# Kernel tuning notes

Hardware: AMD Instinct MI355X
Metric: run time of the kernel (lower is better)

Reference implementation:

```python
import jax, jax.numpy as jnp
import numpy as np

# ---- configuration (matches init_kwargs) ----
IH, IW, IC, OC = 32, 32, 8, 16
KH = KW = 3
STRIDE = (1, 1)
PAD = (1, 1)
DIL = (1, 1)
P = 5                       # num_gp_pts per GP neuron
I_DIM = IC * KH * KW        # 72 = kernel_input_size
OH = (IH + 2 * PAD[0] - DIL[0] * (KH - 1) - 1) // STRIDE[0] + 1
OW = (IW + 2 * PAD[1] - DIL[1] * (KW - 1) - 1) // STRIDE[1] + 1
JITTER = 1e-4


def setup_inputs() -> dict:
    key = jax.random.key(0)
    k1, k2, k3, k4, k5 = jax.random.split(key, 5)
    N = 8
    x_mean = jax.random.normal(k1, (N, IH, IW, IC), jnp.float32)
    # variances must be positive
    x_var = 0.1 + 0.9 * jax.random.uniform(k2, (N, IH, IW, IC), jnp.float32)
    # inducing inputs: spread on [-1,1] with small perturbation (well-conditioned K)
    base = jnp.linspace(-1.0, 1.0, P, dtype=jnp.float32)
    z = base[None, None, :] + 0.05 * jax.random.normal(k3, (OC, I_DIM, P), jnp.float32)
    h = jax.random.normal(k4, (OC, I_DIM, P), jnp.float32)      # inducing outputs
    raw_l = jax.random.uniform(k5, (OC, I_DIM), jnp.float32)    # pre-softplus lengthscale
    return {"x_mean": x_mean, "x_var": x_var, "z": z, "h": h, "raw_l": raw_l}


def im2col(img):
    """[N,IH,IW,C] NHWC -> [N*L, C*KH*KW], torch.nn.Unfold ordering (channel slowest)."""
    x = jnp.transpose(img, (0, 3, 1, 2))  # NCHW, matches the torch transposes
    patches = jax.lax.conv_general_dilated_patches(
        x, (KH, KW), STRIDE, [(PAD[0], PAD[0]), (PAD[1], PAD[1])], rhs_dilation=DIL
    )  # [N, C*KH*KW, OH, OW], feature dim channel-major like torch unfold
    Nb = patches.shape[0]
    return patches.reshape(Nb, I_DIM, OH * OW).transpose(0, 2, 1).reshape(Nb * OH * OW, I_DIM)


def gp_layer(mu, s2, z, h, raw_l):
    """GP-neuron (KAN-style) moment propagation.
    mu, s2: [R, I]; z, h: [O, I, P]; raw_l: [O, I].
    Per neuron (o,i): SE kernel k(a,b)=exp(-(a-b)^2/(2 l^2)), unit signal variance.
    Under x_i ~ N(mu_i, s2_i):
      q_p   = sqrt(l^2/(l^2+s2)) * exp(-(mu-z_p)^2 / (2 (l^2+s2)))   (expected kernel)
      mean  = q . K^{-1} h
      var   = 1 - q . K^{-1} q
    Layer output (KAN sum over inputs): y_o = sum_i f_oi(x_i).
    """
    l2 = jax.nn.softplus(raw_l) ** 2                                  # [O,I]
    dz = z[:, :, :, None] - z[:, :, None, :]                          # [O,I,P,P]
    K = jnp.exp(-0.5 * dz**2 / l2[:, :, None, None]) + JITTER * jnp.eye(P, dtype=mu.dtype)
    Kinv = jnp.linalg.inv(K)                                          # [O,I,P,P] (tiny)
    alpha = jnp.einsum('oipq,oiq->oip', Kinv, h)                      # [O,I,P]

    d = l2[None, :, :, None] + s2[:, None, :, None]                   # [R,O,I,1]
    diff = mu[:, None, :, None] - z[None]                             # [R,O,I,P]
    q = jnp.sqrt(l2[None, :, :, None] / d) * jnp.exp(-0.5 * diff**2 / d)  # [R,O,I,P]

    out_mean = jnp.einsum('roip,oip->ro', q, alpha)                   # [R,O]
    qK = jnp.einsum('roip,oipq->roiq', q, Kinv)                       # [R,O,I,P]
    qKq = jnp.einsum('roiq,roiq->ro', qK, q)                          # [R,O]
    # sum_i (k(x,x) - q K^{-1} q) with k(x,x)=1 -> I - sum_i qKq_i
    out_var = jnp.maximum(jnp.asarray(mu.shape[1], mu.dtype) - qKq, 1e-6)
    return out_mean, out_var


def reference(x_mean, x_var, z, h, raw_l):
    N = x_mean.shape[0]
    mu = im2col(x_mean)                  # [N*L, I]
    s2 = im2col(x_var)                   # [N*L, I]
    m, v = gp_layer(mu, s2, z, h, raw_l)
    # col2im: [N*L, OC] -> [N, OH, OW, OC]
    return m.reshape(N, OH, OW, OC), v.reshape(N, OH, OW, OC)
```

## Files before the change

kernel.cpp:

```cpp
#include <hip/hip_runtime.h>
#include <math.h>

#define OC_N   16
#define I_DIM  72
#define PN     5
#define NEU    (OC_N * I_DIM)
#define NF     32
#define RTOT   8192
#define OUT_HALF (RTOT * OC_N)
#define LOG2E  1.4426950408889634f
#define RLOG2E 0.6931471805599453f

#if __has_builtin(__builtin_amdgcn_rcpf)
#define RCPF(x) __builtin_amdgcn_rcpf(x)
#else
#define RCPF(x) (1.0f / (x))
#endif
#if __has_builtin(__builtin_amdgcn_exp2f)
#define EXP2F(x) __builtin_amdgcn_exp2f(x)
#else
#define EXP2F(x) exp2f(x)
#endif
#if __has_builtin(__builtin_amdgcn_logf)
#define LOG2F(x) __builtin_amdgcn_logf(x)
#else
#define LOG2F(x) log2f(x)
#endif
#if __has_builtin(__builtin_amdgcn_rsqf)
#define RSQF(x) __builtin_amdgcn_rsqf(x)
#else
#define RSQF(x) rsqrtf(x)
#endif


__global__ __launch_bounds__(256) void gp_prep_kernel(
    const float* __restrict__ zin, const float* __restrict__ hin,
    const float* __restrict__ rlin, float* __restrict__ nr) {
  int idx = blockIdx.x * blockDim.x + threadIdx.x;
  if (idx >= NEU) return;
  float x  = rlin[idx];
  float t  = EXP2F(-fabsf(x) * LOG2E);
  float sp = fmaxf(x, 0.0f) + LOG2F(1.0f + t) * RLOG2E;
  float l2 = sp * sp;
  float cexp = -0.5f * LOG2E * RCPF(l2);

  float zz[PN], hh[PN];
#pragma unroll
  for (int p = 0; p < PN; ++p) {
    zz[p] = zin[idx * PN + p];
    hh[p] = hin[idx * PN + p];
  }
  float A[PN][PN], B[PN][PN];
#pragma unroll
  for (int p = 0; p < PN; ++p) {
#pragma unroll
    for (int q = 0; q < PN; ++q) {
      float dz = zz[p] - zz[q];
      A[p][q] = EXP2F(cexp * dz * dz);
      B[p][q] = (p == q) ? 1.0f : 0.0f;
    }
  }
#pragma unroll
  for (int p = 0; p < PN; ++p) A[p][p] += 1e-4f;

#pragma unroll
  for (int c = 0; c < PN; ++c) {
    float pivinv = RCPF(A[c][c]);
#pragma unroll
    for (int j = 0; j < PN; ++j) { A[c][j] *= pivinv; B[c][j] *= pivinv; }
#pragma unroll
    for (int r = 0; r < PN; ++r) {
      if (r == c) continue;
      float f = A[r][c];
#pragma unroll
      for (int j = 0; j < PN; ++j) { A[r][j] -= f * A[c][j]; B[r][j] -= f * B[c][j]; }
    }
  }
  float alpha[PN];
#pragma unroll
  for (int p = 0; p < PN; ++p) {
    float s = 0.0f;
#pragma unroll
    for (int q = 0; q < PN; ++q) s += B[p][q] * hh[q];
    alpha[p] = s;
  }
  float* o = nr + idx * NF;
  o[0] = l2;
  o[1] = 0.0f;
#pragma unroll
  for (int p = 0; p < PN; ++p) {
    o[2 + p]  = zz[p];
    o[7 + p]  = alpha[p];
    o[12 + p] = B[p][p];
  }
  int j = 17;
#pragma unroll
  for (int p = 0; p < PN; ++p)
#pragma unroll
    for (int q = p + 1; q < PN; ++q) o[j++] = 2.0f * B[p][q];
  o[27] = o[28] = o[29] = o[30] = o[31] = 0.0f;
}

__global__ __launch_bounds__(256, 2) void gp_main_kernel(
    const float* __restrict__ xm, const float* __restrict__ xv,
    const float* __restrict__ nr, float2* __restrict__ pmq) {
  const int tx   = threadIdx.x;
  const int lane = tx & 63;
  const int wy   = tx >> 6;
  const int rlo  = lane >> 3;
  const int c    = lane & 7;
  const int k  = blockIdx.z;
  const int kh = k / 3;
  const int kw = k - kh * 3;
  const int o  = blockIdx.y;
  const int rblk = blockIdx.x * 256;

  float P[28];
  {
    const float4* rec4 = (const float4*)(nr + (o * I_DIM + (c * 9 + k)) * NF);
#pragma unroll
    for (int j = 0; j < 7; ++j) *(float4*)&P[4 * j] = rec4[j];
  }
  const float l2 = P[0];

#pragma unroll
  for (int it = 0; it < 8; ++it) {
    const int r8  = rblk + it * 32 + wy * 8;
    const int n   = r8 >> 10;
    const int pix = r8 & 1023;
    const int oh  = pix >> 5;
    const int ow0 = pix & 31;
    const int ih  = oh + kh - 1;
    const int iw  = ow0 + rlo + kw - 1;
    const bool valid = ((unsigned)ih < 32u) & ((unsigned)iw < 32u);
    const int ihc = ih < 0 ? 0 : (ih > 31 ? 31 : ih);
    const int iwc = iw < 0 ? 0 : (iw > 31 ? 31 : iw);
    const int addr = ((n * 32 + ihc) * 32 + iwc) * 8 + c;
    float m = xm[addr];
    float s = xv[addr];
    m = valid ? m : 0.0f;
    s = valid ? s : 0.0f;

    const float d     = l2 + s;
    const float inv_d = RCPF(d);
    const float coef2 = l2 * inv_d;
    const float coef  = coef2 * RSQF(coef2);
    const float el    = -0.72134752044f * inv_d;
    const float d0 = m - P[2];
    const float d1 = m - P[3];
    const float d2 = m - P[4];
    const float d3 = m - P[5];
    const float d4 = m - P[6];
    const float u0 = EXP2F(el * d0 * d0);
    const float u1 = EXP2F(el * d1 * d1);
    const float u2 = EXP2F(el * d2 * d2);
    const float u3 = EXP2F(el * d3 * d3);
    const float u4 = EXP2F(el * d4 * d4);
    const float dotA =
        fmaf(u0, P[7], fmaf(u1, P[8], fmaf(u2, P[9], fmaf(u3, P[10], u4 * P[11]))));
    const float t0 = fmaf(P[12], u0, fmaf(P[17], u1, fmaf(P[18], u2, fmaf(P[19], u3, P[20] * u4))));
    const float t1 = fmaf(P[13], u1, fmaf(P[21], u2, fmaf(P[22], u3, P[23] * u4)));
    const float t2 = fmaf(P[14], u2, fmaf(P[24], u3, P[25] * u4));
    const float t3 = fmaf(P[15], u3, P[26] * u4);
    const float t4 = P[16] * u4;
    const float quad =
        fmaf(u0, t0, fmaf(u1, t1, fmaf(u2, t2, fmaf(u3, t3, u4 * t4))));
    float mean = coef * dotA;
    float qkq  = coef2 * quad;

    mean += __shfl_xor(mean, 1); qkq += __shfl_xor(qkq, 1);
    mean += __shfl_xor(mean, 2); qkq += __shfl_xor(qkq, 2);
    mean += __shfl_xor(mean, 4); qkq += __shfl_xor(qkq, 4);

    if (c == 0)
      pmq[(size_t)(k * OC_N + o) * RTOT + (r8 + rlo)] = make_float2(mean, qkq);
  }
}

__global__ __launch_bounds__(256) void gp_final_kernel(
    const float2* __restrict__ pmq, float* __restrict__ out) {
  const int j = blockIdx.x * 256 + threadIdx.x;
  const int o = j >> 13;
  const int r = j & 8191;
  float m = 0.0f, q = 0.0f;
#pragma unroll
  for (int s = 0; s < 9; ++s) {
    const float2 v = pmq[(size_t)(s * OC_N + o) * RTOT + r];
    m += v.x;
    q += v.y;
  }
  const int i = r * OC_N + o;
  out[i] = m;
  out[OUT_HALF + i] = fmaxf(72.0f - q, 1e-6f);
}

extern "C" void kernel_launch(void* const* d_in, const int* in_sizes, int n_in,
                              void* d_out, int out_size, void* d_ws, size_t ws_size,
                              hipStream_t stream) {
  const float* xm = (const float*)d_in[0];
  const float* xv = (const float*)d_in[1];
  const float* z  = (const float*)d_in[2];
  const float* h  = (const float*)d_in[3];
  const float* rl = (const float*)d_in[4];
  float* out = (float*)d_out;

  float* nr   = (float*)d_ws;
  float2* pmq = (float2*)((char*)d_ws + NEU * NF * 4);

  gp_prep_kernel<<<dim3((NEU + 255) / 256), dim3(256), 0, stream>>>(z, h, rl, nr);

  dim3 grid(RTOT / 256, OC_N, 9);
  gp_main_kernel<<<grid, dim3(256), 0, stream>>>(xm, xv, nr, pmq);

  gp_final_kernel<<<dim3(OUT_HALF / 256), dim3(256), 0, stream>>>(pmq, out);
}
```

Before: 97.63 us.

## Fuse kernel-position reduction into main GP kernel and drop final pass

```diff
diff --git a/kernel.cpp b/kernel.cpp
--- a/kernel.cpp
+++ b/kernel.cpp
@@ -64,16 +64,16 @@
   for (int p = 0; p < PN; ++p) A[p][p] += 1e-4f;
 
 #pragma unroll
-  for (int c = 0; c < PN; ++c) {
-    float pivinv = RCPF(A[c][c]);
-#pragma unroll
-    for (int j = 0; j < PN; ++j) { A[c][j] *= pivinv; B[c][j] *= pivinv; }
+  for (int cc = 0; cc < PN; ++cc) {
+    float pivinv = RCPF(A[cc][cc]);
+#pragma unroll
+    for (int j = 0; j < PN; ++j) { A[cc][j] *= pivinv; B[cc][j] *= pivinv; }
 #pragma unroll
     for (int r = 0; r < PN; ++r) {
-      if (r == c) continue;
-      float f = A[r][c];
-#pragma unroll
-      for (int j = 0; j < PN; ++j) { A[r][j] -= f * A[c][j]; B[r][j] -= f * B[c][j]; }
+      if (r == cc) continue;
+      float f = A[r][cc];
+#pragma unroll
+      for (int j = 0; j < PN; ++j) { A[r][j] -= f * A[cc][j]; B[r][j] -= f * B[cc][j]; }
     }
   }
   float alpha[PN];
@@ -86,7 +86,7 @@
   }
   float* o = nr + idx * NF;
   o[0] = l2;
-  o[1] = 0.0f;
+  o[1] = sp;
 #pragma unroll
   for (int p = 0; p < PN; ++p) {
     o[2 + p]  = zz[p];
@@ -101,97 +101,109 @@
   o[27] = o[28] = o[29] = o[30] = o[31] = 0.0f;
 }
 
-__global__ __launch_bounds__(256, 2) void gp_main_kernel(
+__global__ __launch_bounds__(256, 3) void gp_main_kernel(
     const float* __restrict__ xm, const float* __restrict__ xv,
-    const float* __restrict__ nr, float2* __restrict__ pmq) {
-  const int tx   = threadIdx.x;
-  const int lane = tx & 63;
-  const int wy   = tx >> 6;
-  const int rlo  = lane >> 3;
-  const int c    = lane & 7;
-  const int k  = blockIdx.z;
-  const int kh = k / 3;
-  const int kw = k - kh * 3;
-  const int o  = blockIdx.y;
-  const int rblk = blockIdx.x * 256;
+    const float* __restrict__ nr, float* __restrict__ out) {
+  const int tx    = threadIdx.x;
+  const int lane  = tx & 63;
+  const int wv    = tx >> 6;
+  const int gwave = blockIdx.x * 4 + wv;
+  const int rlo   = lane >> 3;
+  const int c     = lane & 7;
+  const int o     = gwave >> 8;
+  const int rg    = gwave & 255;
+  const int rbase = rg * 32;
+  const int n   = rbase >> 10;
+  const int oh  = (rbase & 1023) >> 5;
+
+  const float* base = nr + (o * I_DIM + c * 9) * NF;
+
+  float macc[4] = {0.f, 0.f, 0.f, 0.f};
+  float qacc[4] = {0.f, 0.f, 0.f, 0.f};
 
   float P[28];
   {
-    const float4* rec4 = (const float4*)(nr + (o * I_DIM + (c * 9 + k)) * NF);
-#pragma unroll
-    for (int j = 0; j < 7; ++j) *(float4*)&P[4 * j] = rec4[j];
-  }
-  const float l2 = P[0];
-
-#pragma unroll
-  for (int it = 0; it < 8; ++it) {
-    const int r8  = rblk + it * 32 + wy * 8;
-    const int n   = r8 >> 10;
-    const int pix = r8 & 1023;
-    const int oh  = pix >> 5;
-    const int ow0 = pix & 31;
-    const int ih  = oh + kh - 1;
-    const int iw  = ow0 + rlo + kw - 1;
-    const bool valid = ((unsigned)ih < 32u) & ((unsigned)iw < 32u);
+    const float4* r4 = (const float4*)base;
+#pragma unroll
+    for (int j = 0; j < 7; ++j) ((float4*)P)[j] = r4[j];
+  }
+
+#pragma unroll 1
+  for (int k = 0; k < 9; ++k) {
+    float Pn[28];
+    if (k < 8) {
+      const float4* r4 = (const float4*)(base + (k + 1) * NF);
+#pragma unroll
+      for (int j = 0; j < 7; ++j) ((float4*)Pn)[j] = r4[j];
+    }
+
+    const int kh = (k * 11) >> 5;
+    const int kw = k - 3 * kh;
+    const int ih = oh + kh - 1;
+    const bool vh = ((unsigned)ih < 32u);
     const int ihc = ih < 0 ? 0 : (ih > 31 ? 31 : ih);
-    const int iwc = iw < 0 ? 0 : (iw > 31 ? 31 : iw);
-    const int addr = ((n * 32 + ihc) * 32 + iwc) * 8 + c;
-    float m = xm[addr];
-    float s = xv[addr];
-    m = valid ? m : 0.0f;
-    s = valid ? s : 0.0f;
-
-    const float d     = l2 + s;
-    const float inv_d = RCPF(d);
-    const float coef2 = l2 * inv_d;
-    const float coef  = coef2 * RSQF(coef2);
-    const float el    = -0.72134752044f * inv_d;
-    const float d0 = m - P[2];
-    const float d1 = m - P[3];
-    const float d2 = m - P[4];
-    const float d3 = m - P[5];
-    const float d4 = m - P[6];
-    const float u0 = EXP2F(el * d0 * d0);
-    const float u1 = EXP2F(el * d1 * d1);
-    const float u2 = EXP2F(el * d2 * d2);
-    const float u3 = EXP2F(el * d3 * d3);
-    const float u4 = EXP2F(el * d4 * d4);
-    const float dotA =
-        fmaf(u0, P[7], fmaf(u1, P[8], fmaf(u2, P[9], fmaf(u3, P[10], u4 * P[11]))));
-    const float t0 = fmaf(P[12], u0, fmaf(P[17], u1, fmaf(P[18], u2, fmaf(P[19], u3, P[20] * u4))));
-    const float t1 = fmaf(P[13], u1, fmaf(P[21], u2, fmaf(P[22], u3, P[23] * u4)));
-    const float t2 = fmaf(P[14], u2, fmaf(P[24], u3, P[25] * u4));
-    const float t3 = fmaf(P[15], u3, P[26] * u4);
-    const float t4 = P[16] * u4;
-    const float quad =
-        fmaf(u0, t0, fmaf(u1, t1, fmaf(u2, t2, fmaf(u3, t3, u4 * t4))));
-    float mean = coef * dotA;
-    float qkq  = coef2 * quad;
-
-    mean += __shfl_xor(mean, 1); qkq += __shfl_xor(qkq, 1);
-    mean += __shfl_xor(mean, 2); qkq += __shfl_xor(qkq, 2);
-    mean += __shfl_xor(mean, 4); qkq += __shfl_xor(qkq, 4);
-
-    if (c == 0)
-      pmq[(size_t)(k * OC_N + o) * RTOT + (r8 + rlo)] = make_float2(mean, qkq);
-  }
-}
-
-__global__ __launch_bounds__(256) void gp_final_kernel(
-    const float2* __restrict__ pmq, float* __restrict__ out) {
-  const int j = blockIdx.x * 256 + threadIdx.x;
-  const int o = j >> 13;
-  const int r = j & 8191;
-  float m = 0.0f, q = 0.0f;
-#pragma unroll
-  for (int s = 0; s < 9; ++s) {
-    const float2 v = pmq[(size_t)(s * OC_N + o) * RTOT + r];
-    m += v.x;
-    q += v.y;
-  }
-  const int i = r * OC_N + o;
-  out[i] = m;
-  out[OUT_HALF + i] = fmaxf(72.0f - q, 1e-6f);
+    const int rowbase = ((n * 32 + ihc) * 32) * 8 + c;
+    const int wo = rlo + kw - 1;
+
+    const float l2 = P[0];
+    const float l1 = P[1];
+
+#pragma unroll
+    for (int it = 0; it < 4; ++it) {
+      const int iw = it * 8 + wo;
+      const bool valid = vh & ((unsigned)iw < 32u);
+      const int iwc = iw < 0 ? 0 : (iw > 31 ? 31 : iw);
+      float m = xm[rowbase + iwc * 8];
+      float s = xv[rowbase + iwc * 8];
+      m = valid ? m : 0.0f;
+      s = valid ? s : 0.0f;
+
+      const float d     = l2 + s;
+      const float irs   = RSQF(d);
+      const float coef  = l1 * irs;
+      const float coef2 = coef * coef;
+      const float el    = -0.72134752044f * (irs * irs);
+      const float d0 = m - P[2];
+      const float d1 = m - P[3];
+      const float d2 = m - P[4];
+      const float d3 = m - P[5];
+      const float d4 = m - P[6];
+      const float u0 = EXP2F(el * d0 * d0);
+      const float u1 = EXP2F(el * d1 * d1);
+      const float u2 = EXP2F(el * d2 * d2);
+      const float u3 = EXP2F(el * d3 * d3);
+      const float u4 = EXP2F(el * d4 * d4);
+      const float dotA =
+          fmaf(u0, P[7], fmaf(u1, P[8], fmaf(u2, P[9], fmaf(u3, P[10], u4 * P[11]))));
+      const float t0 = fmaf(P[12], u0, fmaf(P[17], u1, fmaf(P[18], u2, fmaf(P[19], u3, P[20] * u4))));
+      const float t1 = fmaf(P[13], u1, fmaf(P[21], u2, fmaf(P[22], u3, P[23] * u4)));
+      const float t2 = fmaf(P[14], u2, fmaf(P[24], u3, P[25] * u4));
+      const float t3 = fmaf(P[15], u3, P[26] * u4);
+      const float t4 = P[16] * u4;
+      const float quad =
+          fmaf(u0, t0, fmaf(u1, t1, fmaf(u2, t2, fmaf(u3, t3, u4 * t4))));
+      macc[it] = fmaf(coef, dotA, macc[it]);
+      qacc[it] = fmaf(coef2, quad, qacc[it]);
+    }
+
+    if (k < 8) {
+#pragma unroll
+      for (int j = 0; j < 28; ++j) P[j] = Pn[j];
+    }
+  }
+
+#pragma unroll
+  for (int it = 0; it < 4; ++it) {
+    float mv = macc[it], qv = qacc[it];
+    mv += __shfl_xor(mv, 1); qv += __shfl_xor(qv, 1);
+    mv += __shfl_xor(mv, 2); qv += __shfl_xor(qv, 2);
+    mv += __shfl_xor(mv, 4); qv += __shfl_xor(qv, 4);
+    if (c == 0) {
+      const int r = rbase + it * 8 + rlo;
+      out[r * OC_N + o] = mv;
+      out[OUT_HALF + r * OC_N + o] = fmaxf(72.0f - qv, 1e-6f);
+    }
+  }
 }
 
 extern "C" void kernel_launch(void* const* d_in, const int* in_sizes, int n_in,
@@ -203,14 +215,10 @@
   const float* h  = (const float*)d_in[3];
   const float* rl = (const float*)d_in[4];
   float* out = (float*)d_out;
-
-  float* nr   = (float*)d_ws;
-  float2* pmq = (float2*)((char*)d_ws + NEU * NF * 4);
+  float* nr  = (float*)d_ws;
 
   gp_prep_kernel<<<dim3((NEU + 255) / 256), dim3(256), 0, stream>>>(z, h, rl, nr);
 
-  dim3 grid(RTOT / 256, OC_N, 9);
-  gp_main_kernel<<<grid, dim3(256), 0, stream>>>(xm, xv, nr, pmq);
-
-  gp_final_kernel<<<dim3(OUT_HALF / 256), dim3(256), 0, stream>>>(pmq, out);
+  dim3 grid(1024);
+  gp_main_kernel<<<grid, dim3(256), 0, stream>>>(xm, xv, nr, out);
 }
```

New measurement: 103.2 us. 5.7% more time.
